# Kernel tuning notes

Hardware: AMD Instinct MI355X
Metric: run time of the kernel (lower is better)

## Reference

```python
import jax, jax.numpy as jnp
import numpy as np

D, N_EXP, TOP_K = 2048, 64, 8
B, S = 4, 4096

def setup_inputs() -> dict:
    key = jax.random.key(0)
    k1, k2, k3, k4 = jax.random.split(key, 4)
    hidden_states = jax.random.normal(k1, (B, S, D), dtype=jnp.float32)
    # nn.Linear weights are [out, in]; default init ~ U(-1/sqrt(d), 1/sqrt(d))
    bound = 1.0 / np.sqrt(D)
    W_gate = jax.random.uniform(k2, (N_EXP, D), jnp.float32, -bound, bound)
    W_noise = 0.01 * jax.random.normal(k3, (N_EXP, D), dtype=jnp.float32)
    # training-mode noise (router_step % top_k == 0 path): fixed-seed randn
    noise = jax.random.normal(k4, (B, S, N_EXP), dtype=jnp.float32)
    return {"hidden_states": hidden_states, "W_gate": W_gate,
            "W_noise": W_noise, "noise": noise}

def reference(hidden_states, W_gate, W_noise, noise):
    # logits = h @ W_gate^T  : [B,S,n_exp]
    logits = jnp.einsum('bsd,ed->bse', hidden_states, W_gate)
    scale = jax.nn.softplus(jnp.einsum('bsd,ed->bse', hidden_states, W_noise))
    logits = logits + noise * scale
    gates = jax.nn.softmax(logits, axis=-1)
    vals, inds = jax.lax.top_k(gates, TOP_K)  # sorted desc (torch used sorted=False)
    return vals, inds, gates
```

## Files before the change

### kernel.cpp

```cpp
#include <hip/hip_runtime.h>
#include <math.h>

typedef __attribute__((ext_vector_type(8))) _Float16 half8;
typedef __attribute__((ext_vector_type(4))) float    f32x4;

constexpr int D_DIM = 2048;
constexpr int NEXP  = 64;
constexpr int TOPK  = 8;
constexpr int NTOK  = 16384;
constexpr int TM    = 32;
constexpr int BK    = 64;
constexpr int NCH   = D_DIM / BK;
constexpr int OSTR  = 132;
constexpr int NSTR  = 68;
constexpr float WSCALE  = 4096.0f;
constexpr float INV_WSC = 1.0f / 4096.0f;

__device__ __forceinline__ unsigned short f16b(float x) {
    _Float16 h = (_Float16)x;
    return __builtin_bit_cast(unsigned short, h);
}
__device__ __forceinline__ float f16tof(unsigned short b) {
    return (float)__builtin_bit_cast(_Float16, b);
}

__global__ void prep_w(const float* __restrict__ Wg, const float* __restrict__ Wn,
                       unsigned short* __restrict__ wsB)
{
    const int idx = blockIdx.x * blockDim.x + threadIdx.x;
    const int n   = idx >> 8;
    const int K8  = idx & 255;
    const float* src = (n < 64) ? (Wg + (size_t)n * D_DIM)
                                : (Wn + (size_t)(n - 64) * D_DIM);
    float4 a = *reinterpret_cast<const float4*>(src + K8 * 8);
    float4 b = *reinterpret_cast<const float4*>(src + K8 * 8 + 4);

    float v[8] = {a.x, a.y, a.z, a.w, b.x, b.y, b.z, b.w};
    union { unsigned short u[8]; half8 s; } H, L;
#pragma unroll
    for (int j = 0; j < 8; ++j) {
        float xs = v[j] * WSCALE;
        unsigned short h = f16b(xs);
        H.u[j] = h;
        L.u[j] = f16b(xs - f16tof(h));
    }
    const int l = ((K8 & 3) * 16) + (n & 15);
    const size_t base = (size_t)(K8 >> 2) * 8192 + (size_t)(n >> 4) * 1024 + (size_t)l * 8;
    *reinterpret_cast<half8*>(wsB + base)       = H.s;
    *reinterpret_cast<half8*>(wsB + base + 512) = L.s;
}

__global__ __launch_bounds__(512, 4)
void noisy_topk_router(const float* __restrict__ hs,
                       const unsigned short* __restrict__ wsB,
                       const float* __restrict__ nz,
                       float* __restrict__ out)
{
    __shared__ __align__(16) char smem[16896 + 8704];
    unsigned short* stage  = reinterpret_cast<unsigned short*>(smem);
    float*          logits = reinterpret_cast<float*>(smem);
    float*          ldsN   = reinterpret_cast<float*>(smem + 16896);

    const int tid  = threadIdx.x;
    const int lane = tid & 63;
    const int w    = tid >> 6;
    const int t0   = blockIdx.x * TM;

    const int r  = tid >> 4;
    const int k4 = (tid & 15) * 4;
    const float* hrow = hs + (size_t)(t0 + r) * D_DIM + k4;
    const int ks_s = k4 >> 5;
    const int kk   = k4 & 31;
    const int j0   = kk >> 3;
    const int pos  = kk & 7;
    const int mt_s = r >> 4;
    const int m_s  = r & 15;
    const int wroff = (mt_s * 2 + ks_s) * 512 + (j0 * 16 + m_s) * 8 + pos;

    f32x4 accH0[2], accH1[2], accX[2];
#pragma unroll
    for (int mt = 0; mt < 2; ++mt) {
        accH0[mt] = (f32x4){0.f, 0.f, 0.f, 0.f};
        accH1[mt] = (f32x4){0.f, 0.f, 0.f, 0.f};
        accX[mt]  = (f32x4){0.f, 0.f, 0.f, 0.f};
    }

    auto cvt_write = [&](float4 v, unsigned short* buf) {
        float p[4] = {v.x, v.y, v.z, v.w};
        unsigned int Hp[2], Lp[2];
#pragma unroll
        for (int q = 0; q < 2; ++q) {
            unsigned short h0 = f16b(p[2*q]);
            unsigned short h1 = f16b(p[2*q+1]);
            unsigned short l0 = f16b(p[2*q]   - f16tof(h0));
            unsigned short l1 = f16b(p[2*q+1] - f16tof(h1));
            Hp[q] = (unsigned int)h0 | ((unsigned int)h1 << 16);
            Lp[q] = (unsigned int)l0 | ((unsigned int)l1 << 16);
        }
        *reinterpret_cast<uint2*>(buf + wroff)        = make_uint2(Hp[0], Hp[1]);
        *reinterpret_cast<uint2*>(buf + 2048 + wroff) = make_uint2(Lp[0], Lp[1]);
    };

    cvt_write(*reinterpret_cast<const float4*>(hrow), stage);
    __syncthreads();

    for (int c = 0; c < NCH; ++c) {
        float4 pf;
        if (c + 1 < NCH)
            pf = *reinterpret_cast<const float4*>(hrow + (c + 1) * BK);

        const unsigned short* sb = stage + (c & 1) * 4096;

#pragma unroll
        for (int ks = 0; ks < 2; ++ks) {
            const unsigned short* bp = wsB + (size_t)(2 * c + ks) * 8192
                                           + (size_t)w * 1024 + (size_t)lane * 8;
            half8 bhi = *reinterpret_cast<const half8*>(bp);
            half8 blo = *reinterpret_cast<const half8*>(bp + 512);
#pragma unroll
            for (int mt = 0; mt < 2; ++mt) {
                half8 ahi = *reinterpret_cast<const half8*>(sb + (mt * 2 + ks) * 512 + lane * 8);
                half8 alo = *reinterpret_cast<const half8*>(sb + 2048 + (mt * 2 + ks) * 512 + lane * 8);
                if (ks == 0)
                    accH0[mt] = __builtin_amdgcn_mfma_f32_16x16x32_f16(ahi, bhi, accH0[mt], 0, 0, 0);
                else
                    accH1[mt] = __builtin_amdgcn_mfma_f32_16x16x32_f16(ahi, bhi, accH1[mt], 0, 0, 0);
                accX[mt] = __builtin_amdgcn_mfma_f32_16x16x32_f16(ahi, blo, accX[mt], 0, 0, 0);
                accX[mt] = __builtin_amdgcn_mfma_f32_16x16x32_f16(alo, bhi, accX[mt], 0, 0, 0);
            }
        }

        if (c + 1 < NCH)
            cvt_write(pf, stage + ((c + 1) & 1) * 4096);
        __syncthreads();
    }

    {
        const int colb = w * 16 + (lane & 15);
        const int rowb = (lane >> 4) * 4;
#pragma unroll
        for (int mt = 0; mt < 2; ++mt)
#pragma unroll
            for (int rr = 0; rr < 4; ++rr)
                logits[(mt * 16 + rowb + rr) * OSTR + colb] =
                    (accH0[mt][rr] + accH1[mt][rr] + accX[mt][rr]) * INV_WSC;
    }
    {
        const int rr = tid >> 4;
        const int cc = tid & 15;
        float4 v = *reinterpret_cast<const float4*>(nz + (size_t)(t0 + rr) * NEXP + cc * 4);
        *reinterpret_cast<float4*>(&ldsN[rr * NSTR + cc * 4]) = v;
    }
    __syncthreads();

    if (tid < TM) {
        const int tok = t0 + tid;
        float l[NEXP];
        float mx = -3.0e38f;
#pragma unroll
        for (int e = 0; e < NEXP; ++e) {
            float gsc = logits[tid * OSTR + e];
            float nl  = logits[tid * OSTR + 64 + e];
            float sp  = fmaxf(nl, 0.0f) + log1pf(expf(-fabsf(nl)));
            float le  = fmaf(ldsN[tid * NSTR + e], sp, gsc);
            l[e] = le;
            mx = fmaxf(mx, le);
        }
        float sum = 0.0f;
#pragma unroll
        for (int e = 0; e < NEXP; ++e) { float p = expf(l[e] - mx); l[e] = p; sum += p; }
        float inv = 1.0f / sum;
#pragma unroll
        for (int e = 0; e < NEXP; ++e) l[e] *= inv;

#pragma unroll
        for (int e = 0; e < NEXP; ++e) logits[tid * OSTR + e] = l[e];

        float* vout = out + (size_t)tok * TOPK;
        float* iout = out + (size_t)NTOK * TOPK + (size_t)tok * TOPK;
#pragma unroll
        for (int p = 0; p < TOPK; ++p) {
            float m = -1.0f; int mi = 0;
#pragma unroll
            for (int e = 0; e < NEXP; ++e) {
                bool gt = l[e] > m;
                m  = gt ? l[e] : m;
                mi = gt ? e : mi;
            }
            vout[p] = m;
            iout[p] = (float)mi;
#pragma unroll
            for (int e = 0; e < NEXP; ++e) l[e] = (e == mi) ? -1.0f : l[e];
        }
    }
    __syncthreads();

    {
        const int rr = tid >> 4;
        const int cc = tid & 15;
        float* gout = out + (size_t)NTOK * TOPK * 2;
        float4 v = *reinterpret_cast<const float4*>(&logits[rr * OSTR + cc * 4]);
        *reinterpret_cast<float4*>(&gout[(size_t)(t0 + rr) * NEXP + cc * 4]) = v;
    }
}

extern "C" void kernel_launch(void* const* d_in, const int* in_sizes, int n_in,
                              void* d_out, int out_size, void* d_ws, size_t ws_size,
                              hipStream_t stream) {
    const float* hs = (const float*)d_in[0];
    const float* Wg = (const float*)d_in[1];
    const float* Wn = (const float*)d_in[2];
    const float* nz = (const float*)d_in[3];
    float* out = (float*)d_out;
    unsigned short* wsB = (unsigned short*)d_ws;

    prep_w<<<64, 512, 0, stream>>>(Wg, Wn, wsB);
    noisy_topk_router<<<NTOK / TM, 512, 0, stream>>>(hs, wsB, nz, out);
}
```

Baseline: 243.8 us.

## Retile router GEMM to 16-token blocks with per-wave 32-expert tiles and swizzled LDS

Shrinks the token tile from 32 to 16 and the block from 512 to 256 threads. Each of the four waves now owns two 16-expert column tiles and keeps the weight fragments for a 128-wide K chunk in registers. The staging layout uses XOR-swizzled offsets to avoid LDS bank conflicts, and each thread converts eight floats per chunk. The aim is more blocks for latency hiding, fewer barriers per K, and more MFMA work per A-fragment load. The cost is more register pressure and weight traffic read from global or L2 twice as often per token.

After: 265.5 us. 1.09x slower.

```diff
diff --git a/kernel.cpp b/kernel.cpp
--- a/kernel.cpp
+++ b/kernel.cpp
@@ -8,9 +8,9 @@
 constexpr int NEXP  = 64;
 constexpr int TOPK  = 8;
 constexpr int NTOK  = 16384;
-constexpr int TM    = 32;
-constexpr int BK    = 64;
-constexpr int NCH   = D_DIM / BK;
+constexpr int TM    = 16;
+constexpr int BK    = 128;
+constexpr int NREG  = D_DIM / BK;
 constexpr int OSTR  = 132;
 constexpr int NSTR  = 68;
 constexpr float WSCALE  = 4096.0f;
@@ -50,100 +50,108 @@
     *reinterpret_cast<half8*>(wsB + base + 512) = L.s;
 }
 
-__global__ __launch_bounds__(512, 4)
+__global__ __launch_bounds__(256, 4)
 void noisy_topk_router(const float* __restrict__ hs,
                        const unsigned short* __restrict__ wsB,
                        const float* __restrict__ nz,
                        float* __restrict__ out)
 {
-    __shared__ __align__(16) char smem[16896 + 8704];
+    __shared__ __align__(16) char smem[16384];
     unsigned short* stage  = reinterpret_cast<unsigned short*>(smem);
     float*          logits = reinterpret_cast<float*>(smem);
-    float*          ldsN   = reinterpret_cast<float*>(smem + 16896);
+    float*          ldsN   = reinterpret_cast<float*>(smem + 8448);
 
     const int tid  = threadIdx.x;
     const int lane = tid & 63;
     const int w    = tid >> 6;
     const int t0   = blockIdx.x * TM;
 
-    const int r  = tid >> 4;
-    const int k4 = (tid & 15) * 4;
-    const float* hrow = hs + (size_t)(t0 + r) * D_DIM + k4;
-    const int ks_s = k4 >> 5;
-    const int kk   = k4 & 31;
-    const int j0   = kk >> 3;
-    const int pos  = kk & 7;
-    const int mt_s = r >> 4;
-    const int m_s  = r & 15;
-    const int wroff = (mt_s * 2 + ks_s) * 512 + (j0 * 16 + m_s) * 8 + pos;
-
-    f32x4 accH0[2], accH1[2], accX[2];
-#pragma unroll
-    for (int mt = 0; mt < 2; ++mt) {
-        accH0[mt] = (f32x4){0.f, 0.f, 0.f, 0.f};
-        accH1[mt] = (f32x4){0.f, 0.f, 0.f, 0.f};
-        accX[mt]  = (f32x4){0.f, 0.f, 0.f, 0.f};
-    }
-
-    auto cvt_write = [&](float4 v, unsigned short* buf) {
-        float p[4] = {v.x, v.y, v.z, v.w};
-        unsigned int Hp[2], Lp[2];
-#pragma unroll
-        for (int q = 0; q < 2; ++q) {
-            unsigned short h0 = f16b(p[2*q]);
-            unsigned short h1 = f16b(p[2*q+1]);
-            unsigned short l0 = f16b(p[2*q]   - f16tof(h0));
-            unsigned short l1 = f16b(p[2*q+1] - f16tof(h1));
-            Hp[q] = (unsigned int)h0 | ((unsigned int)h1 << 16);
-            Lp[q] = (unsigned int)l0 | ((unsigned int)l1 << 16);
-        }
-        *reinterpret_cast<uint2*>(buf + wroff)        = make_uint2(Hp[0], Hp[1]);
-        *reinterpret_cast<uint2*>(buf + 2048 + wroff) = make_uint2(Lp[0], Lp[1]);
+    const int row  = tid >> 4;
+    const int oct  = tid & 15;
+    const int ks_s = oct >> 2;
+    const int j0_s = oct & 3;
+    const float* hrow = hs + (size_t)(t0 + row) * D_DIM + oct * 8;
+    const int lane_w = j0_s * 16 + row;
+    const int wr_hi  = (ks_s * 64 + (lane_w ^ (j0_s << 1) ^ ks_s)) * 8;
+
+    const int l_sw = lane ^ ((lane >> 4) << 1);
+    int aoff[4];
+#pragma unroll
+    for (int ks = 0; ks < 4; ++ks)
+        aoff[ks] = (ks * 64 + (l_sw ^ ks)) * 8;
+
+    f32x4 accH[2][2], accX[2];
+#pragma unroll
+    for (int nt = 0; nt < 2; ++nt) {
+        accH[0][nt] = (f32x4){0.f, 0.f, 0.f, 0.f};
+        accH[1][nt] = (f32x4){0.f, 0.f, 0.f, 0.f};
+        accX[nt]    = (f32x4){0.f, 0.f, 0.f, 0.f};
+    }
+
+    auto cvt_write = [&](float4 v0, float4 v1, unsigned short* buf) {
+        float x[8] = {v0.x, v0.y, v0.z, v0.w, v1.x, v1.y, v1.z, v1.w};
+        union { unsigned short u[8]; half8 s; } H, L;
+#pragma unroll
+        for (int j = 0; j < 8; ++j) {
+            unsigned short h = f16b(x[j]);
+            H.u[j] = h;
+            L.u[j] = f16b(x[j] - f16tof(h));
+        }
+        *reinterpret_cast<half8*>(buf + wr_hi)        = H.s;
+        *reinterpret_cast<half8*>(buf + 2048 + wr_hi) = L.s;
     };
 
-    cvt_write(*reinterpret_cast<const float4*>(hrow), stage);
+    cvt_write(*reinterpret_cast<const float4*>(hrow),
+              *reinterpret_cast<const float4*>(hrow + 4), stage);
     __syncthreads();
 
-    for (int c = 0; c < NCH; ++c) {
-        float4 pf;
-        if (c + 1 < NCH)
-            pf = *reinterpret_cast<const float4*>(hrow + (c + 1) * BK);
+    const unsigned short* bwave = wsB + (size_t)(2 * w) * 1024 + (size_t)lane * 8;
+
+    for (int c = 0; c < NREG; ++c) {
+        half8 bh[4][2], bl[4][2];
+#pragma unroll
+        for (int ks = 0; ks < 4; ++ks) {
+            const unsigned short* bp = bwave + (size_t)(c * 4 + ks) * 8192;
+            bh[ks][0] = *reinterpret_cast<const half8*>(bp);
+            bl[ks][0] = *reinterpret_cast<const half8*>(bp + 512);
+            bh[ks][1] = *reinterpret_cast<const half8*>(bp + 1024);
+            bl[ks][1] = *reinterpret_cast<const half8*>(bp + 1536);
+        }
+        float4 p0, p1;
+        if (c + 1 < NREG) {
+            p0 = *reinterpret_cast<const float4*>(hrow + (c + 1) * BK);
+            p1 = *reinterpret_cast<const float4*>(hrow + (c + 1) * BK + 4);
+        }
 
         const unsigned short* sb = stage + (c & 1) * 4096;
-
-#pragma unroll
-        for (int ks = 0; ks < 2; ++ks) {
-            const unsigned short* bp = wsB + (size_t)(2 * c + ks) * 8192
-                                           + (size_t)w * 1024 + (size_t)lane * 8;
-            half8 bhi = *reinterpret_cast<const half8*>(bp);
-            half8 blo = *reinterpret_cast<const half8*>(bp + 512);
-#pragma unroll
-            for (int mt = 0; mt < 2; ++mt) {
-                half8 ahi = *reinterpret_cast<const half8*>(sb + (mt * 2 + ks) * 512 + lane * 8);
-                half8 alo = *reinterpret_cast<const half8*>(sb + 2048 + (mt * 2 + ks) * 512 + lane * 8);
-                if (ks == 0)
-                    accH0[mt] = __builtin_amdgcn_mfma_f32_16x16x32_f16(ahi, bhi, accH0[mt], 0, 0, 0);
-                else
-                    accH1[mt] = __builtin_amdgcn_mfma_f32_16x16x32_f16(ahi, bhi, accH1[mt], 0, 0, 0);
-                accX[mt] = __builtin_amdgcn_mfma_f32_16x16x32_f16(ahi, blo, accX[mt], 0, 0, 0);
-                accX[mt] = __builtin_amdgcn_mfma_f32_16x16x32_f16(alo, bhi, accX[mt], 0, 0, 0);
+#pragma unroll
+        for (int ks = 0; ks < 4; ++ks) {
+            half8 ahi = *reinterpret_cast<const half8*>(sb + aoff[ks]);
+            half8 alo = *reinterpret_cast<const half8*>(sb + 2048 + aoff[ks]);
+#pragma unroll
+            for (int nt = 0; nt < 2; ++nt) {
+                accH[ks & 1][nt] = __builtin_amdgcn_mfma_f32_16x16x32_f16(ahi, bh[ks][nt], accH[ks & 1][nt], 0, 0, 0);
+                accX[nt]         = __builtin_amdgcn_mfma_f32_16x16x32_f16(ahi, bl[ks][nt], accX[nt], 0, 0, 0);
+                accX[nt]         = __builtin_amdgcn_mfma_f32_16x16x32_f16(alo, bh[ks][nt], accX[nt], 0, 0, 0);
             }
         }
 
-        if (c + 1 < NCH)
-            cvt_write(pf, stage + ((c + 1) & 1) * 4096);
+        if (c + 1 < NREG)
+            cvt_write(p0, p1, stage + ((c + 1) & 1) * 4096);
         __syncthreads();
     }
 
     {
-        const int colb = w * 16 + (lane & 15);
         const int rowb = (lane >> 4) * 4;
-#pragma unroll
-        for (int mt = 0; mt < 2; ++mt)
-#pragma unroll
-            for (int rr = 0; rr < 4; ++rr)
-                logits[(mt * 16 + rowb + rr) * OSTR + colb] =
-                    (accH0[mt][rr] + accH1[mt][rr] + accX[mt][rr]) * INV_WSC;
+        const int colw = lane & 15;
+#pragma unroll
+        for (int nt = 0; nt < 2; ++nt) {
+            const int colb = (2 * w + nt) * 16 + colw;
+#pragma unroll
+            for (int r = 0; r < 4; ++r)
+                logits[(rowb + r) * OSTR + colb] =
+                    (accH[0][nt][r] + accH[1][nt][r] + accX[nt][r]) * INV_WSC;
+        }
     }
     {
         const int rr = tid >> 4;
@@ -215,5 +223,5 @@
     unsigned short* wsB = (unsigned short*)d_ws;
 
     prep_w<<<64, 512, 0, stream>>>(Wg, Wn, wsB);
-    noisy_topk_router<<<NTOK / TM, 512, 0, stream>>>(hs, wsB, nz, out);
-}
+    noisy_topk_router<<<NTOK / TM, 256, 0, stream>>>(hs, wsB, nz, out);
+}
```
